# Kernel optimization log

Hardware: AMD Instinct MI355X
Metric: run time of the kernel (lower is better)

The kernel has to match this reference:

```python
import jax, jax.numpy as jnp
import numpy as np

NUM_LAYERS = 4
EPS = 1e-8


def setup_inputs() -> dict:
    key = jax.random.key(0)
    ks = jax.random.split(key, 7)
    N, D, H = 8192, 1024, 4096
    return {
        "x": jax.random.normal(ks[0], (N, D), jnp.float32),
        "fc1_W": jax.random.normal(ks[1], (H, D), jnp.float32) * 0.02,
        "fc1_b": jax.random.normal(ks[2], (H,), jnp.float32) * 0.02,
        "fc2_W": jax.random.normal(ks[3], (D, H), jnp.float32) * 0.02,
        "fc2_b": jax.random.normal(ks[4], (D,), jnp.float32) * 0.02,
        "comp_W": jax.random.normal(ks[5], (NUM_LAYERS + 1, D, D), jnp.float32) * 0.03,
        "comp_b": jax.random.normal(ks[6], (NUM_LAYERS + 1, D), jnp.float32) * 0.03,
    }


def _block(x, fc1_W, fc1_b, fc2_W, fc2_b):
    # fc2(dropout(fc1(x))) in eval mode; relu is defined but never applied
    h = x @ fc1_W.T + fc1_b
    return h @ fc2_W.T + fc2_b


def _compute_loss(z, W, b):
    # out = Linear(z); per-row cosine_similarity(out_i.unsqueeze(1), out_i.unsqueeze(0))
    # reduces broadcast dim 1 -> vector c[j] = out[j]*sum(out) / max(|out[j]|*sqrt(y)*||out||, eps)
    # which torch broadcasts into constant rows of a [y,y] matrix; the
    # abs-diff accumulation over batch rows is then rank-1.
    out = z @ W.T + b                                # [N, y]
    y = out.shape[-1]
    S = out.sum(-1, keepdims=True)                   # [N, 1]
    n2 = jnp.sqrt((out * out).sum(-1, keepdims=True))  # [N, 1] row norms
    n1 = jnp.abs(out) * jnp.sqrt(jnp.asarray(y, out.dtype))  # [N, y]
    c = out * S / jnp.maximum(n1 * n2, EPS)          # [N, y]
    D = jnp.abs(c[1:] - c[:-1]).sum(0)               # [y]
    return jnp.broadcast_to(D, (y, y))               # [y, y]


def reference(x, fc1_W, fc1_b, fc2_W, fc2_b, comp_W, comp_b):
    inv = _block(x, fc1_W, fc1_b, fc2_W, fc2_b)
    loss = _compute_loss(inv, comp_W[0], comp_b[0])
    nxt = x - inv
    inv_total = inv
    for i in range(1, NUM_LAYERS + 1):
        inv_new = _block(nxt, fc1_W, fc1_b, fc2_W, fc2_b)
        inv_total = inv_total + inv_new
        loss = loss + _compute_loss(inv_new, comp_W[i], comp_b[i])
        nxt = nxt - inv_new
    return inv_total, nxt, loss
```

## Files before the change

### kernel.cpp

```cpp
#include <hip/hip_runtime.h>
#include <hip/hip_bf16.h>


#define NR 8192
#define DD 1024
#define HH 4096
#define NL 5
#define MSZ (DD * DD)

using bf16 = __hip_bfloat16;
typedef __attribute__((ext_vector_type(8))) short bf16x8;
typedef __attribute__((ext_vector_type(4))) float f32x4;


__device__ __forceinline__ void cvt4(const float* __restrict__ in, bf16* __restrict__ out, int i) {
  float4 v = ((const float4*)in)[i];
  union { bf16 b[4]; uint2 u; } u;
  u.b[0] = __float2bfloat16(v.x); u.b[1] = __float2bfloat16(v.y);
  u.b[2] = __float2bfloat16(v.z); u.b[3] = __float2bfloat16(v.w);
  ((uint2*)out)[i] = u.u;
}

#define NX4 (NR * DD / 4)
#define NF4 (DD * HH / 4)
#define NC4 (NL * MSZ / 4)
#define NS4 ((NL * DD + 2 * NL * NR) / 4)
#define NE4 (DD)

__global__ void prep_kernel(const float* __restrict__ x, const float* __restrict__ fc2_W,
                            const float* __restrict__ comp_W,
                            bf16* __restrict__ x_bf, bf16* __restrict__ fc2_bf,
                            bf16* __restrict__ compW_bf,
                            float* __restrict__ stats, float* __restrict__ ebuf) {
  int i = blockIdx.x * 256 + threadIdx.x;
  const int stride = gridDim.x * 256;
  const int total = NX4 + NF4 + NC4 + NS4 + NE4;
  const float4 z4 = {0.f, 0.f, 0.f, 0.f};
  for (; i < total; i += stride) {
    if (i < NX4) cvt4(x, x_bf, i);
    else if (i < NX4 + NF4) cvt4(fc2_W, fc2_bf, i - NX4);
    else if (i < NX4 + NF4 + NC4) cvt4(comp_W, compW_bf, i - NX4 - NF4);
    else if (i < NX4 + NF4 + NC4 + NS4) ((float4*)stats)[i - NX4 - NF4 - NC4] = z4;
    else ((float4*)ebuf)[i - NX4 - NF4 - NC4 - NS4] = z4;
  }
}

__global__ void transpose_cvt_kernel(const float* __restrict__ in, bf16* __restrict__ out) {
  __shared__ bf16 tile[64][74];
  int c0 = blockIdx.x * 64;
  int r0 = blockIdx.y * 64;
  int col = threadIdx.x & 63;
  int row4 = threadIdx.x >> 6;
  #pragma unroll
  for (int j = 0; j < 16; ++j) {
    int r = row4 * 16 + j;
    tile[r][col] = __float2bfloat16(in[(size_t)(r0 + r) * DD + c0 + col]);
  }
  __syncthreads();
  #pragma unroll
  for (int j = 0; j < 16; ++j) {
    int r = row4 * 16 + j;
    out[(size_t)(c0 + r) * HH + r0 + col] = tile[col][r];
  }
}

__global__ void cvec_kernel(const float* __restrict__ fc1_b, const float* __restrict__ fc2_W,
                            const float* __restrict__ fc2_b, float* __restrict__ c) {
  int j = blockIdx.x;
  float s = 0.f;
  for (int k = threadIdx.x; k < HH; k += 256) s += fc1_b[k] * fc2_W[(size_t)j * HH + k];
  for (int o = 32; o; o >>= 1) s += __shfl_down(s, o);
  __shared__ float red[4];
  if ((threadIdx.x & 63) == 0) red[threadIdx.x >> 6] = s;
  __syncthreads();
  if (threadIdx.x == 0) c[j] = red[0] + red[1] + red[2] + red[3] + fc2_b[j];
}

__global__ void mbuild_kernel(const float* __restrict__ Cp,
                              bf16* __restrict__ M, bf16* __restrict__ T, bf16* __restrict__ Tt) {
  __shared__ float tile[64][65];
  int n0 = blockIdx.x * 64, m0 = blockIdx.y * 64;
  int tn = threadIdx.x & 63, tm4 = threadIdx.x >> 6;
  #pragma unroll
  for (int j = 0; j < 16; ++j) {
    int m = tm4 * 16 + j;
    size_t idx = (size_t)(m0 + m) * DD + n0 + tn;
    float v = Cp[idx] + Cp[MSZ + idx] + Cp[2 * MSZ + idx] + Cp[3 * MSZ + idx];
    tile[m][tn] = v;
    float d = ((m0 + m) == (n0 + tn)) ? 1.f : 0.f;
    M[idx] = __float2bfloat16(v);
    T[idx] = __float2bfloat16(d - v);
  }
  __syncthreads();
  #pragma unroll
  for (int j = 0; j < 16; ++j) {
    int r = tm4 * 16 + j;
    float v = tile[tn][r];
    size_t idx = (size_t)(n0 + r) * DD + m0 + tn;
    float d = ((n0 + r) == (m0 + tn)) ? 1.f : 0.f;
    Tt[idx] = __float2bfloat16(d - v);
  }
}

__global__ void gemv4_kernel(const float* __restrict__ c, const bf16* __restrict__ Pw,
                             float* __restrict__ ebuf) {
  const int z = blockIdx.y;
  const int j = blockIdx.x * 256 + threadIdx.x;
  const bf16* P = Pw + (size_t)z * MSZ + j;
  const int k0 = blockIdx.z * 256;
  float s = 0.f;
  #pragma unroll 8
  for (int k = k0; k < k0 + 256; ++k) s += c[k] * __bfloat162float(P[(size_t)k * DD]);
  atomicAdd(&ebuf[z * DD + j], s);
}

__global__ void biasall_kernel(const float* __restrict__ cvec, const float* __restrict__ ebuf,
                               const float* __restrict__ comp_W, const float* __restrict__ comp_b,
                               float* __restrict__ biasall) {
  int z = blockIdx.y, j = blockIdx.x;
  if (z == 0) {
    if (threadIdx.x == 0)
      biasall[j] = cvec[j] + ebuf[j] + ebuf[DD + j] + ebuf[2 * DD + j] + ebuf[3 * DD + j];
    return;
  }
  int i = z - 1;
  const float* e = (i == 0) ? cvec : ebuf + (size_t)(i - 1) * DD;
  const float* wr = comp_W + (size_t)i * MSZ + (size_t)j * DD;
  float s = 0.f;
  for (int k = threadIdx.x; k < DD; k += 256) s += e[k] * wr[k];
  for (int o = 32; o; o >>= 1) s += __shfl_down(s, o);
  __shared__ float red[4];
  if ((threadIdx.x & 63) == 0) red[threadIdx.x >> 6] = s;
  __syncthreads();
  if (threadIdx.x == 0)
    biasall[(size_t)z * DD + j] = red[0] + red[1] + red[2] + red[3] + comp_b[(size_t)i * DD + j];
}


__device__ __forceinline__ void async16(const bf16* g, bf16* l) {
  __builtin_amdgcn_global_load_lds(
      (const __attribute__((address_space(1))) void*)g,
      (__attribute__((address_space(3))) void*)l, 16, 0, 0);
}

__device__ __forceinline__ void gemm_core64(
    const bf16* __restrict__ A, const bf16* __restrict__ B,
    int kBeg, int kEnd, int lda, int ldb, int bm, int bn,
    bf16* As, bf16* Bs, f32x4 acc[2][2])
{
  const int tid  = threadIdx.x;
  const int lane = tid & 63;
  const int wave = tid >> 6;
  const int wm = (wave & 1) * 32;
  const int wn = (wave >> 1) * 32;
  const int lr = lane >> 3;
  const int lcol = ((lane & 7) ^ lr) * 8;
  const bf16* gA = A + (size_t)(bm + wave * 16 + lr) * lda + lcol;
  const bf16* gB = B + (size_t)(bn + wave * 16 + lr) * ldb + lcol;
  bf16* lA = As + wave * 16 * 64;
  bf16* lB = Bs + wave * 16 * 64;

  for (int k0 = kBeg; k0 < kEnd; k0 += 64) {
    #pragma unroll
    for (int it = 0; it < 2; ++it) {
      async16(gA + (size_t)(it * 8) * lda + k0, lA + it * 8 * 64);
      async16(gB + (size_t)(it * 8) * ldb + k0, lB + it * 8 * 64);
    }
    __syncthreads();
    #pragma unroll
    for (int ks = 0; ks < 2; ++ks) {
      bf16x8 av[2], bv[2];
      #pragma unroll
      for (int i = 0; i < 2; ++i) {
        const int rr = i * 16 + (lane & 15);
        const int cc = ((ks * 4 + (lane >> 4)) ^ (lane & 7)) * 8;
        av[i] = *(const bf16x8*)(As + (wm + rr) * 64 + cc);
        bv[i] = *(const bf16x8*)(Bs + (wn + rr) * 64 + cc);
      }
      #pragma unroll
      for (int i = 0; i < 2; ++i)
        #pragma unroll
        for (int j = 0; j < 2; ++j)
          acc[i][j] = __builtin_amdgcn_mfma_f32_16x16x32_bf16(av[i], bv[j], acc[i][j], 0, 0, 0);
    }
    __syncthreads();
  }
}

#define GEMM_PROLOGUE64 \
  alignas(16) __shared__ bf16 As[64 * 64]; \
  alignas(16) __shared__ bf16 Bs[64 * 64]; \
  f32x4 acc[2][2] = {}; \
  const int lane = threadIdx.x & 63; \
  const int wm = ((threadIdx.x >> 6) & 1) * 32; \
  const int wn = ((threadIdx.x >> 6) >> 1) * 32;

__global__ __launch_bounds__(256, 4)
void gemm_splitk64(const bf16* __restrict__ A, const bf16* __restrict__ B, float* __restrict__ Cp) {
  GEMM_PROLOGUE64
  const int bm = blockIdx.y * 64, bn = blockIdx.x * 64;
  const int kb = blockIdx.z * (HH / 4);
  gemm_core64(A, B, kb, kb + HH / 4, HH, HH, bm, bn, As, Bs, acc);
  float* C = Cp + (size_t)blockIdx.z * MSZ;
  #pragma unroll
  for (int i = 0; i < 2; ++i)
    #pragma unroll
    for (int j = 0; j < 2; ++j) {
      const int col = bn + wn + j * 16 + (lane & 15);
      #pragma unroll
      for (int r = 0; r < 4; ++r) {
        const int row = bm + wm + i * 16 + (lane >> 4) * 4 + r;
        C[(size_t)row * DD + col] = acc[i][j][r];
      }
    }
}

__global__ __launch_bounds__(256, 4)
void gemm_dual64(const bf16* __restrict__ A, const bf16* __restrict__ B,
                 bf16* __restrict__ Ct, bf16* __restrict__ Cn) {
  GEMM_PROLOGUE64
  const int bm = blockIdx.y * 64, bn = blockIdx.x * 64;
  gemm_core64(A, B, 0, DD, DD, DD, bm, bn, As, Bs, acc);
  #pragma unroll
  for (int i = 0; i < 2; ++i)
    #pragma unroll
    for (int j = 0; j < 2; ++j) {
      const int col = bn + wn + j * 16 + (lane & 15);
      const int row0 = bm + wm + i * 16 + (lane >> 4) * 4;
      union { bf16 b[4]; uint2 u; } pk;
      #pragma unroll
      for (int r = 0; r < 4; ++r) {
        bf16 v = __float2bfloat16(acc[i][j][r]);
        pk.b[r] = v;
        Cn[(size_t)(row0 + r) * DD + col] = v;
      }
      *(uint2*)(&Ct[(size_t)col * DD + row0]) = pk.u;
    }
}

__global__ __launch_bounds__(256, 4)
void gemm_b64(const bf16* __restrict__ A0, long astr, const bf16* __restrict__ B0, long bstr,
              bf16* __restrict__ C0, long cstr) {
  GEMM_PROLOGUE64
  const int z = blockIdx.z;
  const bf16* A = A0 + (size_t)z * astr;
  const bf16* B = B0 + (size_t)z * bstr;
  bf16* C = C0 + (size_t)z * cstr;
  const int bm = blockIdx.y * 64, bn = blockIdx.x * 64;
  gemm_core64(A, B, 0, DD, DD, DD, bm, bn, As, Bs, acc);
  #pragma unroll
  for (int i = 0; i < 2; ++i)
    #pragma unroll
    for (int j = 0; j < 2; ++j) {
      const int col = bn + wn + j * 16 + (lane & 15);
      #pragma unroll
      for (int r = 0; r < 4; ++r) {
        const int row = bm + wm + i * 16 + (lane >> 4) * 4 + r;
        C[(size_t)row * DD + col] = __float2bfloat16(acc[i][j][r]);
      }
    }
}

__global__ __launch_bounds__(256, 4)
void gemm_t5_64(const bf16* __restrict__ A, const bf16* __restrict__ B,
                const bf16* __restrict__ Pw, bf16* __restrict__ Dl, bf16* __restrict__ Bbig0) {
  GEMM_PROLOGUE64
  const int bm = blockIdx.y * 64, bn = blockIdx.x * 64;
  gemm_core64(A, B, 0, DD, DD, DD, bm, bn, As, Bs, acc);
  #pragma unroll
  for (int i = 0; i < 2; ++i)
    #pragma unroll
    for (int j = 0; j < 2; ++j) {
      const int col = bn + wn + j * 16 + (lane & 15);
      const int row0 = bm + wm + i * 16 + (lane >> 4) * 4;
      union { bf16 b[4]; uint2 u; } pk;
      #pragma unroll
      for (int r = 0; r < 4; ++r) {
        const size_t idx = (size_t)(row0 + r) * DD + col;
        const float t1 = __bfloat162float(Pw[idx]);
        const float t2 = __bfloat162float(Pw[MSZ + idx]);
        const float t3 = __bfloat162float(Pw[2 * MSZ + idx]);
        const float t4 = __bfloat162float(Pw[3 * MSZ + idx]);
        const float t5 = acc[i][j][r];
        Dl[idx]           = __float2bfloat16(t1 - t2);
        Dl[MSZ + idx]     = __float2bfloat16(t2 - t3);
        Dl[2 * MSZ + idx] = __float2bfloat16(t3 - t4);
        Dl[3 * MSZ + idx] = __float2bfloat16(t4 - t5);
        pk.b[r] = __float2bfloat16((((row0 + r) == col) ? 1.f : 0.f) - t5);
      }
      *(uint2*)(&Bbig0[(size_t)col * DD + row0]) = pk.u;
    }
}


__global__ __launch_bounds__(512, 2)
void gemm_main256(const bf16* __restrict__ A, const bf16* __restrict__ Bb,
                  const float* __restrict__ biasall, const bf16* __restrict__ xb,
                  float* __restrict__ invtot, float* __restrict__ nxtf,
                  unsigned long long* __restrict__ sgn,
                  float* __restrict__ Srow, float* __restrict__ Qrow) {
  __shared__ bf16 Ls[65536];
  const int tid  = threadIdx.x;
  const int lane = tid & 63;
  const int w    = tid >> 6;
  const int wr   = w >> 2, wc = w & 3;
  const int gbn  = blockIdx.x * 256;
  const int bm   = blockIdx.y * 256;
  const int zm   = gbn >> 10;
  const int cbase = gbn & (DD - 1);
  const bf16* Bz = Bb + (size_t)zm * MSZ;

  f32x4 acc[8][4] = {};

  const int lr  = lane >> 3;
  const int lc  = ((lane & 7) ^ lr) * 8;
  const int l15 = lane & 15;
  const int cc0 = (((lane >> 4)    ) ^ (lane & 7)) * 8;
  const int cc1 = (((lane >> 4) + 4) ^ (lane & 7)) * 8;

  auto ldsHalf = [&](int buf, int mat, int half) -> bf16* {
    return Ls + (((buf << 2) | (mat << 1) | half) << 13);
  };
  auto stageHalf = [&](int buf, int mat, int half, int k0) {
    const bf16* g = (mat == 0)
      ? A  + (size_t)(bm    + half * 128 + w * 16 + lr) * DD + k0 + lc
      : Bz + (size_t)(cbase + half * 128 + w * 16 + lr) * DD + k0 + lc;
    bf16* d = ldsHalf(buf, mat, half) + w * 1024;
    async16(g, d);
    async16(g + (size_t)8 * DD, d + 512);
  };

  stageHalf(0, 0, 0, 0); stageHalf(0, 0, 1, 0);
  stageHalf(0, 1, 0, 0); stageHalf(0, 1, 1, 0);
  asm volatile("s_waitcnt vmcnt(0)" ::: "memory");
  __builtin_amdgcn_sched_barrier(0);
  __builtin_amdgcn_s_barrier();
  __builtin_amdgcn_sched_barrier(0);

  #pragma unroll 2
  for (int t = 0; t < 16; ++t) {
    const int p = t & 1;
    const bf16* Ah = ldsHalf(p, 0, wr);
    const bf16* Bh = ldsHalf(p, 1, wc >> 1);
    const int brl = (wc & 1) * 64;
    const int k1 = (t + 1) * 64;
    #pragma unroll
    for (int ph = 0; ph < 4; ++ph) {
      const int qm = ph & 1, qn = ph >> 1;
      if (ph == 0) {
        if (t < 15) stageHalf(p ^ 1, 0, 0, k1);
        __builtin_amdgcn_sched_barrier(0);
        if (t < 15) { asm volatile("s_waitcnt vmcnt(2)" ::: "memory"); }
        else        { asm volatile("s_waitcnt vmcnt(0)" ::: "memory"); }
        __builtin_amdgcn_sched_barrier(0);
        __builtin_amdgcn_s_barrier();
        __builtin_amdgcn_sched_barrier(0);
      } else {
        if (t < 15) stageHalf(p ^ 1, ph >> 1, ph & 1, k1);
      }
      bf16x8 av[4][2], bv[2][2];
      #pragma unroll
      for (int i2 = 0; i2 < 4; ++i2) {
        const bf16* ap = Ah + (qm * 64 + i2 * 16 + l15) * 64;
        av[i2][0] = *(const bf16x8*)(ap + cc0);
        av[i2][1] = *(const bf16x8*)(ap + cc1);
      }
      #pragma unroll
      for (int j2 = 0; j2 < 2; ++j2) {
        const bf16* bp = Bh + (brl + qn * 32 + j2 * 16 + l15) * 64;
        bv[j2][0] = *(const bf16x8*)(bp + cc0);
        bv[j2][1] = *(const bf16x8*)(bp + cc1);
      }
      __builtin_amdgcn_s_setprio(1);
      #pragma unroll
      for (int i2 = 0; i2 < 4; ++i2)
        #pragma unroll
        for (int j2 = 0; j2 < 2; ++j2) {
          acc[qm * 4 + i2][qn * 2 + j2] = __builtin_amdgcn_mfma_f32_16x16x32_bf16(
              av[i2][0], bv[j2][0], acc[qm * 4 + i2][qn * 2 + j2], 0, 0, 0);
          acc[qm * 4 + i2][qn * 2 + j2] = __builtin_amdgcn_mfma_f32_16x16x32_bf16(
              av[i2][1], bv[j2][1], acc[qm * 4 + i2][qn * 2 + j2], 0, 0, 0);
        }
      __builtin_amdgcn_s_setprio(0);
      __builtin_amdgcn_sched_barrier(0);
      __builtin_amdgcn_s_barrier();
      __builtin_amdgcn_sched_barrier(0);
    }
  }

  if (zm == 0) {
    #pragma unroll
    for (int i = 0; i < 8; ++i)
      #pragma unroll
      for (int j = 0; j < 4; ++j) {
        const int col = cbase + wc * 64 + j * 16 + l15;
        const float bj = biasall[col];
        #pragma unroll
        for (int r = 0; r < 4; ++r) {
          const int row = bm + wr * 128 + i * 16 + (lane >> 4) * 4 + r;
          const float v = acc[i][j][r] + bj;
          const size_t idx = (size_t)row * DD + col;
          invtot[idx] = v;
          nxtf[idx] = __bfloat162float(xb[idx]) - v;
        }
      }
  } else {
    const int z = zm - 1;
    const int cg = (cbase >> 6) + wc;
    unsigned long long keep0 = 0ULL, keep1 = 0ULL;
    #pragma unroll
    for (int i = 0; i < 8; ++i) {
      float sv[4] = {0.f, 0.f, 0.f, 0.f}, qv[4] = {0.f, 0.f, 0.f, 0.f};
      #pragma unroll
      for (int r = 0; r < 4; ++r) {
        unsigned long long bal[4];
        #pragma unroll
        for (int j = 0; j < 4; ++j) {
          const float bj = biasall[gbn + wc * 64 + j * 16 + l15];
          const float v = acc[i][j][r] + bj;
          bal[j] = __ballot(v < 0.f);
          sv[r] += v; qv[r] += v * v;
        }
        #pragma unroll
        for (int rg = 0; rg < 4; ++rg) {
          const unsigned long long wv =
              (((bal[0] >> (rg * 16)) & 0xFFFFULL)      ) |
              (((bal[1] >> (rg * 16)) & 0xFFFFULL) << 16) |
              (((bal[2] >> (rg * 16)) & 0xFFFFULL) << 32) |
              (((bal[3] >> (rg * 16)) & 0xFFFFULL) << 48);
          const int tl = i * 8 + rg * 2 + (r >> 1);
          if (lane == tl) { if (r & 1) keep1 = wv; else keep0 = wv; }
        }
      }
      #pragma unroll
      for (int r = 0; r < 4; ++r) {
        float s = sv[r], q = qv[r];
        #pragma unroll
        for (int off = 1; off < 16; off <<= 1) { s += __shfl_xor(s, off); q += __shfl_xor(q, off); }
        if (l15 == 0) {
          const int row = bm + wr * 128 + i * 16 + (lane >> 4) * 4 + r;
          atomicAdd(&Srow[(size_t)z * NR + row], s);
          atomicAdd(&Qrow[(size_t)z * NR + row], q);
        }
      }
    }
    const int row0 = bm + wr * 128 + lane * 2;
    sgn[(((size_t)z * NR + row0) << 4) + cg] = keep0;
    sgn[(((size_t)z * NR + row0 + 1) << 4) + cg] = keep1;
  }
}


__global__ void losssign_kernel(const unsigned long long* __restrict__ sgn,
                                const float* __restrict__ Srow, const float* __restrict__ Qrow,
                                float* __restrict__ Dtot) {
  const int z = blockIdx.y;
  const int cg = blockIdx.x;
  const int n0 = blockIdx.z * 1024;
  __shared__ float rsh[1025];
  const float* S = Srow + (size_t)z * NR;
  const float* Q = Qrow + (size_t)z * NR;
  for (int t = threadIdx.x; t < 1025; t += 256) {
    int n = n0 + t; if (n > NR - 1) n = NR - 1;
    rsh[t] = S[n] * rsqrtf(Q[n]) * 0.03125f;
  }
  __syncthreads();
  const int c = threadIdx.x & 63;
  const int q = threadIdx.x >> 6;
  const int col = cg * 64 + c;
  const int ns = n0 + q * 256;
  int ne = ns + 256; if (ne > NR - 1) ne = NR - 1;

  auto cval = [&](int n) -> float {
    const unsigned long long wv = sgn[(((size_t)z * NR + n) << 4) + cg];
    const float rv = rsh[n - n0];
    return ((wv >> c) & 1ULL) ? -rv : rv;
  };

  float d = 0.f;
  float cprev = cval(ns);
  for (int n = ns + 1; n <= ne; ++n) {
    const float cn = cval(n);
    d += fabsf(cn - cprev);
    cprev = cn;
  }
  atomicAdd(&Dtot[z * DD + col], d);
}

__global__ void writeloss_kernel(const float* __restrict__ Dtot, float* __restrict__ out) {
  int idx = blockIdx.x * 256 + threadIdx.x;
  int j = idx & (DD - 1);
  out[idx] = Dtot[j] + Dtot[DD + j] + Dtot[2 * DD + j] + Dtot[3 * DD + j] + Dtot[4 * DD + j];
}


extern "C" void kernel_launch(void* const* d_in, const int* in_sizes, int n_in,
                              void* d_out, int out_size, void* d_ws, size_t ws_size,
                              hipStream_t stream) {
  const float* x      = (const float*)d_in[0];
  const float* fc1_W  = (const float*)d_in[1];
  const float* fc1_b  = (const float*)d_in[2];
  const float* fc2_W  = (const float*)d_in[3];
  const float* fc2_b  = (const float*)d_in[4];
  const float* comp_W = (const float*)d_in[5];
  const float* comp_b = (const float*)d_in[6];

  float* invtot  = (float*)d_out;
  float* nxtf    = invtot + (size_t)NR * DD;
  float* lossout = invtot + (size_t)2 * NR * DD;

  char* w = (char*)d_ws;
  auto alloc = [&](size_t bytes) { char* p = w; w += (bytes + 255) & ~(size_t)255; return p; };
  bf16* x_bf     = (bf16*)alloc((size_t)NR * DD * 2);
  bf16* fc1T_bf  = (bf16*)alloc((size_t)DD * HH * 2);
  bf16* fc2_bf   = (bf16*)alloc((size_t)DD * HH * 2);
  bf16* compW_bf = (bf16*)alloc((size_t)NL * MSZ * 2);
  bf16* Dbank    = (bf16*)alloc((size_t)5 * MSZ * 2);
  bf16* M_bf = Dbank;
  bf16* Dl   = Dbank + MSZ;
  bf16* Tt_buf   = (bf16*)alloc((size_t)2 * MSZ * 2);
  bf16* Pw       = (bf16*)alloc((size_t)4 * MSZ * 2);
  bf16* Bbig     = (bf16*)alloc((size_t)6 * MSZ * 2);
  unsigned long long* sgn = (unsigned long long*)alloc((size_t)NL * NR * 16 * 8);
  float* Cp      = (float*)alloc((size_t)4 * MSZ * 4);
  float* cvec    = (float*)alloc(DD * 4);
  float* ebuf    = (float*)alloc((size_t)4 * DD * 4);
  float* biasall = (float*)alloc((size_t)6 * DD * 4);
  float* stats   = (float*)alloc((size_t)(NL * DD + 2 * NL * NR) * 4);
  float* Dtot = stats;
  float* Srow = stats + NL * DD;
  float* Qrow = Srow + (size_t)NL * NR;
  (void)ws_size; (void)in_sizes; (void)n_in; (void)out_size;

  prep_kernel<<<2048, 256, 0, stream>>>(x, fc2_W, comp_W, x_bf, fc2_bf, compW_bf, stats, ebuf);
  transpose_cvt_kernel<<<dim3(DD / 64, HH / 64), 256, 0, stream>>>(fc1_W, fc1T_bf);
  cvec_kernel<<<DD, 256, 0, stream>>>(fc1_b, fc2_W, fc2_b, cvec);

  gemm_splitk64<<<dim3(16, 16, 4), 256, 0, stream>>>(fc1T_bf, fc2_bf, Cp);
  mbuild_kernel<<<dim3(16, 16), 256, 0, stream>>>(Cp, M_bf, Pw, Tt_buf);
  gemm_dual64<<<dim3(16, 16), 256, 0, stream>>>(Pw, Tt_buf, Tt_buf + MSZ, Pw + MSZ);
  gemm_b64<<<dim3(16, 16, 2), 256, 0, stream>>>(Pw + MSZ, 0, Tt_buf, MSZ, Pw + 2 * MSZ, MSZ);
  gemm_t5_64<<<dim3(16, 16), 256, 0, stream>>>(Pw + 3 * MSZ, Tt_buf, Pw, Dl, Bbig);
  gemv4_kernel<<<dim3(4, 4, 4), 256, 0, stream>>>(cvec, Pw, ebuf);
  biasall_kernel<<<dim3(DD, 6), 256, 0, stream>>>(cvec, ebuf, comp_W, comp_b, biasall);
  gemm_b64<<<dim3(16, 16, NL), 256, 0, stream>>>(compW_bf, MSZ, Dbank, MSZ, Bbig + MSZ, MSZ);

  gemm_main256<<<dim3(6 * DD / 256, NR / 256), 512, 0, stream>>>(
      x_bf, Bbig, biasall, x_bf, invtot, nxtf, sgn, Srow, Qrow);

  losssign_kernel<<<dim3(16, NL, 8), 256, 0, stream>>>(sgn, Srow, Qrow, Dtot);
  writeloss_kernel<<<MSZ / 256, 256, 0, stream>>>(Dtot, lossout);
}
```

Before: 484.7 us.

## Simplify GEMM main loop to one barrier per K-tile with upfront prefetch

Restructures the K loop: all four async stage copies for the next tile are issued at the start of each iteration, and compute walks the two k-halves over the full 8x4 accumulator tile. There is one vmcnt(0) wait plus barrier per iteration instead of four per-phase barriers. This cuts synchronization overhead and reloads of LDS fragments. In exchange it loses the fine-grained interleaving of loads with MFMA phases and raises register pressure (8 A and 4 B fragments live at once).

```diff
diff --git a/kernel.cpp b/kernel.cpp
--- a/kernel.cpp
+++ b/kernel.cpp
@@ -340,52 +340,35 @@
   #pragma unroll 2
   for (int t = 0; t < 16; ++t) {
     const int p = t & 1;
+    if (t < 15) {
+      const int k1 = (t + 1) * 64;
+      stageHalf(p ^ 1, 0, 0, k1); stageHalf(p ^ 1, 0, 1, k1);
+      stageHalf(p ^ 1, 1, 0, k1); stageHalf(p ^ 1, 1, 1, k1);
+    }
     const bf16* Ah = ldsHalf(p, 0, wr);
-    const bf16* Bh = ldsHalf(p, 1, wc >> 1);
-    const int brl = (wc & 1) * 64;
-    const int k1 = (t + 1) * 64;
-    #pragma unroll
-    for (int ph = 0; ph < 4; ++ph) {
-      const int qm = ph & 1, qn = ph >> 1;
-      if (ph == 0) {
-        if (t < 15) stageHalf(p ^ 1, 0, 0, k1);
-        __builtin_amdgcn_sched_barrier(0);
-        if (t < 15) { asm volatile("s_waitcnt vmcnt(2)" ::: "memory"); }
-        else        { asm volatile("s_waitcnt vmcnt(0)" ::: "memory"); }
-        __builtin_amdgcn_sched_barrier(0);
-        __builtin_amdgcn_s_barrier();
-        __builtin_amdgcn_sched_barrier(0);
-      } else {
-        if (t < 15) stageHalf(p ^ 1, ph >> 1, ph & 1, k1);
-      }
-      bf16x8 av[4][2], bv[2][2];
-      #pragma unroll
-      for (int i2 = 0; i2 < 4; ++i2) {
-        const bf16* ap = Ah + (qm * 64 + i2 * 16 + l15) * 64;
-        av[i2][0] = *(const bf16x8*)(ap + cc0);
-        av[i2][1] = *(const bf16x8*)(ap + cc1);
-      }
-      #pragma unroll
-      for (int j2 = 0; j2 < 2; ++j2) {
-        const bf16* bp = Bh + (brl + qn * 32 + j2 * 16 + l15) * 64;
-        bv[j2][0] = *(const bf16x8*)(bp + cc0);
-        bv[j2][1] = *(const bf16x8*)(bp + cc1);
-      }
+    const bf16* Bh = ldsHalf(p, 1, wc >> 1) + (wc & 1) * 64 * 64;
+    #pragma unroll
+    for (int kk = 0; kk < 2; ++kk) {
+      const int cc = kk ? cc1 : cc0;
+      bf16x8 av[8], bv[4];
+      #pragma unroll
+      for (int i = 0; i < 8; ++i)
+        av[i] = *(const bf16x8*)(Ah + (i * 16 + l15) * 64 + cc);
+      #pragma unroll
+      for (int j = 0; j < 4; ++j)
+        bv[j] = *(const bf16x8*)(Bh + (j * 16 + l15) * 64 + cc);
       __builtin_amdgcn_s_setprio(1);
       #pragma unroll
-      for (int i2 = 0; i2 < 4; ++i2)
+      for (int i = 0; i < 8; ++i)
         #pragma unroll
-        for (int j2 = 0; j2 < 2; ++j2) {
-          acc[qm * 4 + i2][qn * 2 + j2] = __builtin_amdgcn_mfma_f32_16x16x32_bf16(
-              av[i2][0], bv[j2][0], acc[qm * 4 + i2][qn * 2 + j2], 0, 0, 0);
-          acc[qm * 4 + i2][qn * 2 + j2] = __builtin_amdgcn_mfma_f32_16x16x32_bf16(
-              av[i2][1], bv[j2][1], acc[qm * 4 + i2][qn * 2 + j2], 0, 0, 0);
-        }
+        for (int j = 0; j < 4; ++j)
+          acc[i][j] = __builtin_amdgcn_mfma_f32_16x16x32_bf16(av[i], bv[j], acc[i][j], 0, 0, 0);
       __builtin_amdgcn_s_setprio(0);
-      __builtin_amdgcn_sched_barrier(0);
-      __builtin_amdgcn_s_barrier();
-      __builtin_amdgcn_sched_barrier(0);
-    }
+    }
+    asm volatile("s_waitcnt vmcnt(0)" ::: "memory");
+    __builtin_amdgcn_sched_barrier(0);
+    __builtin_amdgcn_s_barrier();
+    __builtin_amdgcn_sched_barrier(0);
   }
 
   if (zm == 0) {
```

Result: slower. 505.6 us (+4.3%).
